# Kernel optimization log

Hardware: AMD Instinct MI355X
Metric: run time of the kernel (lower is better)

The kernel has to match this reference:

```python
import jax, jax.numpy as jnp
import numpy as np

V, C, BLK = 32000, 512, 2048
B, T = 4, 2048
EPS = 1e-5


def _layernorm(x, g, b):
    mu = jnp.mean(x, axis=-1, keepdims=True)
    var = jnp.mean(jnp.square(x - mu), axis=-1, keepdims=True)
    return (x - mu) * jax.lax.rsqrt(var + EPS) * g + b


def setup_inputs() -> dict:
    key = jax.random.key(0)
    ks = jax.random.split(key, 16)
    s = 0.02
    return {
        "idx": jax.random.randint(ks[0], (B, T), 0, V),
        "targets": jax.random.randint(ks[1], (B, T), 0, V),
        "tok_emb": jax.random.normal(ks[2], (V, C), jnp.float32) * s,
        "pos_emb": jax.random.normal(ks[3], (BLK, C), jnp.float32) * s,
        "Wk": jax.random.normal(ks[4], (C, C), jnp.float32) * s,
        "Wq": jax.random.normal(ks[5], (C, C), jnp.float32) * s,
        "Wv": jax.random.normal(ks[6], (C, C), jnp.float32) * s,
        "W1": jax.random.normal(ks[7], (4 * C, C), jnp.float32) * s,
        "b1": jnp.zeros((4 * C,), jnp.float32),
        "W2": jax.random.normal(ks[8], (C, 4 * C), jnp.float32) * s,
        "b2": jnp.zeros((C,), jnp.float32),
        "g1": jnp.ones((C,), jnp.float32),
        "beta1": jnp.zeros((C,), jnp.float32),
        "g2": jnp.ones((C,), jnp.float32),
        "beta2": jnp.zeros((C,), jnp.float32),
        "Wlm": jax.random.normal(ks[9], (V, C), jnp.float32) * s,
        "blm": jnp.zeros((V,), jnp.float32),
    }


def reference(idx, targets, tok_emb, pos_emb, Wk, Wq, Wv, W1, b1, W2, b2,
              g1, beta1, g2, beta2, Wlm, blm):
    # embeddings
    x = tok_emb[idx] + pos_emb[:T]  # [B,T,C]
    # single-head causal self-attention (dropout = identity, eval mode)
    h = _layernorm(x, g1, beta1)
    q = jnp.einsum('btc,dc->btd', h, Wq)
    k = jnp.einsum('btc,dc->btd', h, Wk)
    v = jnp.einsum('btc,dc->btd', h, Wv)
    wei = jnp.einsum('btd,bsd->bts', q, k) * (C ** -0.5)  # [B,T,T]
    mask = jnp.tril(jnp.ones((T, T), bool))
    wei = jnp.where(mask, wei, -jnp.inf)
    wei = jax.nn.softmax(wei, axis=-1)
    x = x + jnp.einsum('bts,bsd->btd', wei, v)
    # FFN
    h2 = _layernorm(x, g2, beta2)
    ff = jax.nn.relu(jnp.einsum('btc,fc->btf', h2, W1) + b1)
    x = x + jnp.einsum('btf,cf->btc', ff, W2) + b2
    # lm head + cross-entropy
    logits = (jnp.einsum('btc,vc->btv', x, Wlm) + blm).reshape(B * T, V)
    logp = jax.nn.log_softmax(logits, axis=-1)
    loss = -jnp.mean(jnp.take_along_axis(logp, targets.reshape(-1, 1), axis=1))
    return logits, loss
```

## Files before the change

### kernel.cpp

```cpp
#include <hip/hip_runtime.h>

typedef __bf16 bf16;
typedef __bf16 bf16x8 __attribute__((ext_vector_type(8)));
typedef float  f32x4  __attribute__((ext_vector_type(4)));

#define NB 4
#define NT 2048
#define NC 512
#define NV 32000
#define NROWS (NB*NT)
#define NCHUNK (NV/256)
#define LNEPS 1e-5f
#define SMEM_B 131072

static __device__ __forceinline__ void load_lds16(const bf16* g, char* l) {
  __builtin_amdgcn_global_load_lds(
      (const __attribute__((address_space(1))) void*)g,
      (__attribute__((address_space(3))) void*)l, 16, 0, 0);
}

static __device__ __forceinline__ void bar() {
  asm volatile("" ::: "memory");
  __builtin_amdgcn_s_barrier();
  asm volatile("" ::: "memory");
}

__global__ __launch_bounds__(256)
void cvt_kernel(const float* __restrict__ in, bf16* __restrict__ out, int n8) {
  long i = (long)blockIdx.x * 256 + threadIdx.x;
  long stride = (long)gridDim.x * 256;
  for (; i < n8; i += stride) {
    const float* p = in + i * 8;
    f32x4 a = *(const f32x4*)p;
    f32x4 b = *(const f32x4*)(p + 4);
    bf16x8 o;
    o[0]=(bf16)a.x; o[1]=(bf16)a.y; o[2]=(bf16)a.z; o[3]=(bf16)a.w;
    o[4]=(bf16)b.x; o[5]=(bf16)b.y; o[6]=(bf16)b.z; o[7]=(bf16)b.w;
    *(bf16x8*)(out + i*8) = o;
  }
}

__global__ __launch_bounds__(64)
void embed_ln_kernel(const int* __restrict__ idx, const float* __restrict__ tok,
                     const float* __restrict__ pos, const float* __restrict__ gw,
                     const float* __restrict__ bw,
                     float* __restrict__ x0, bf16* __restrict__ h1) {
  int row = blockIdx.x;
  int t = row & (NT-1);
  int id = idx[row];
  int lane = threadIdx.x;
  const float* tr = tok + (long)id*NC + lane*8;
  const float* pr = pos + (long)t*NC + lane*8;
  f32x4 a0 = *(const f32x4*)tr, a1 = *(const f32x4*)(tr+4);
  f32x4 p0 = *(const f32x4*)pr, p1 = *(const f32x4*)(pr+4);
  f32x4 r0 = a0 + p0, r1 = a1 + p1;
  float* o = x0 + (long)row*NC + lane*8;
  *(f32x4*)o = r0; *(f32x4*)(o+4) = r1;
  float v[8] = {r0.x,r0.y,r0.z,r0.w,r1.x,r1.y,r1.z,r1.w};
  float s = 0.f;
  #pragma unroll
  for (int j=0;j<8;++j) s += v[j];
  #pragma unroll
  for (int m=32;m>=1;m>>=1) s += __shfl_xor(s, m);
  float mu = s * (1.f/NC);
  float sq = 0.f;
  #pragma unroll
  for (int j=0;j<8;++j) { v[j] -= mu; sq += v[j]*v[j]; }
  #pragma unroll
  for (int m=32;m>=1;m>>=1) sq += __shfl_xor(sq, m);
  float rs = rsqrtf(sq * (1.f/NC) + LNEPS);
  const float* gp = gw + lane*8;
  const float* bp = bw + lane*8;
  f32x4 g0 = *(const f32x4*)gp, g1 = *(const f32x4*)(gp+4);
  f32x4 b0 = *(const f32x4*)bp, b1 = *(const f32x4*)(bp+4);
  float gg[8] = {g0.x,g0.y,g0.z,g0.w,g1.x,g1.y,g1.z,g1.w};
  float bb[8] = {b0.x,b0.y,b0.z,b0.w,b1.x,b1.y,b1.z,b1.w};
  bf16x8 oo;
  #pragma unroll
  for (int j=0;j<8;++j) oo[j] = (bf16)(v[j]*rs*gg[j] + bb[j]);
  *(bf16x8*)(h1 + (long)row*NC + lane*8) = oo;
}

__global__ __launch_bounds__(64)
void ln_kernel(const float* __restrict__ x, const float* __restrict__ gw,
               const float* __restrict__ bw, bf16* __restrict__ out) {
  int row = blockIdx.x;
  int lane = threadIdx.x;
  const float* xr = x + (long)row*NC + lane*8;
  f32x4 a = *(const f32x4*)xr;
  f32x4 b = *(const f32x4*)(xr+4);
  float v[8] = {a.x,a.y,a.z,a.w,b.x,b.y,b.z,b.w};
  float s = 0.f;
  #pragma unroll
  for (int j=0;j<8;++j) s += v[j];
  #pragma unroll
  for (int m=32;m>=1;m>>=1) s += __shfl_xor(s, m);
  float mu = s * (1.f/NC);
  float sq = 0.f;
  #pragma unroll
  for (int j=0;j<8;++j) { v[j] -= mu; sq += v[j]*v[j]; }
  #pragma unroll
  for (int m=32;m>=1;m>>=1) sq += __shfl_xor(sq, m);
  float rs = rsqrtf(sq * (1.f/NC) + LNEPS);
  const float* gp = gw + lane*8;
  const float* bp = bw + lane*8;
  f32x4 g0 = *(const f32x4*)gp, g1 = *(const f32x4*)(gp+4);
  f32x4 b0 = *(const f32x4*)bp, b1 = *(const f32x4*)(bp+4);
  float gg[8] = {g0.x,g0.y,g0.z,g0.w,g1.x,g1.y,g1.z,g1.w};
  float bb[8] = {b0.x,b0.y,b0.z,b0.w,b1.x,b1.y,b1.z,b1.w};
  bf16x8 o;
  #pragma unroll
  for (int j=0;j<8;++j) o[j] = (bf16)(v[j]*rs*gg[j] + bb[j]);
  *(bf16x8*)(out + (long)row*NC + lane*8) = o;
}

__global__ __launch_bounds__(256)
void transpose_kernel(const bf16* __restrict__ v, long ldv, bf16* __restrict__ vt) {
  __shared__ bf16 tile[64][66];
  int b = blockIdx.z;
  int t0 = blockIdx.x*64, c0 = blockIdx.y*64;
  int tid = threadIdx.x;
  int r = tid >> 2, ch = (tid & 3) * 16;
  const bf16* src = v + ((long)b*NT + t0 + r)*ldv + c0 + ch;
  #pragma unroll
  for (int i=0;i<16;++i) tile[r][ch+i] = src[i];
  __syncthreads();
  bf16x8 o0, o1;
  #pragma unroll
  for (int i=0;i<8;++i) o0[i] = tile[ch+i][r];
  #pragma unroll
  for (int i=0;i<8;++i) o1[i] = tile[ch+8+i][r];
  bf16* dst = vt + ((long)b*NC + c0 + r)*NT + t0 + ch;
  *(bf16x8*)dst = o0;
  *(bf16x8*)(dst+8) = o1;
}

__global__ __launch_bounds__(256)
void softmax_kernel(float* __restrict__ S) {
  const int row = blockIdx.x;
  const int t = row & (NT-1);
  const int tid = threadIdx.x;
  float* sr = S + (long)row*NT;
  bf16* pr = (bf16*)S + (long)row*(2*NT);
  const float scale = 0.044194173824159216f;
  f32x4 v0 = *(const f32x4*)(sr + tid*8);
  f32x4 v1 = *(const f32x4*)(sr + tid*8 + 4);
  float v[8] = {v0.x,v0.y,v0.z,v0.w,v1.x,v1.y,v1.z,v1.w};
  int cb = tid*8;
  float mx = -1e30f;
  #pragma unroll
  for (int j=0;j<8;++j) {
    v[j] = (cb + j <= t) ? v[j]*scale : -1e30f;
    mx = fmaxf(mx, v[j]);
  }
  __shared__ float redm[4];
  #pragma unroll
  for (int m=32;m>=1;m>>=1) mx = fmaxf(mx, __shfl_xor(mx, m));
  if ((tid & 63) == 0) redm[tid>>6] = mx;
  __syncthreads();
  mx = fmaxf(fmaxf(redm[0],redm[1]), fmaxf(redm[2],redm[3]));
  float e[8]; float s = 0.f;
  #pragma unroll
  for (int j=0;j<8;++j) { e[j] = (cb + j <= t) ? __expf(v[j]-mx) : 0.f; s += e[j]; }
  __shared__ float reds[4];
  #pragma unroll
  for (int m=32;m>=1;m>>=1) s += __shfl_xor(s, m);
  if ((tid & 63) == 0) reds[tid>>6] = s;
  __syncthreads();
  s = reds[0]+reds[1]+reds[2]+reds[3];
  float inv = 1.f/s;
  bf16x8 o;
  #pragma unroll
  for (int j=0;j<8;++j) o[j] = (bf16)(e[j]*inv);
  *(bf16x8*)(pr + cb) = o;
}

enum { EPI_F32=0, EPI_BF16=1, EPI_BIAS_RELU_BF16=2, EPI_BIAS_RES_BF16=3, EPI_RES_F32=4, EPI_LMHEAD=5 };

template<int EPI, bool CAUSAL=false, bool KLIMIT=false, bool SWAP=false>
__global__ __launch_bounds__(512,2)
void gemm256(const bf16* __restrict__ A, const bf16* __restrict__ B, int nkt,
             long lda, long ldb, long sAb, long sBb,
             float* __restrict__ outf, bf16* __restrict__ outb, long ldo, long sOb,
             const float* __restrict__ bias,
             const float* __restrict__ res, long ldr, long sRb,
             float* __restrict__ pmax, float* __restrict__ psum) {
  extern __shared__ char smem[];
  int bn, bm;
  if constexpr (SWAP) { bm = blockIdx.x; bn = blockIdx.y; }
  else               { bn = blockIdx.x; bm = blockIdx.y; }
  const int bz = blockIdx.z;
  if constexpr (CAUSAL) { if (bn > bm) return; }
  int nkt_eff = nkt;
  if constexpr (KLIMIT) { int c = (bm+1)*4; if (c < nkt_eff) nkt_eff = c; }

  const int tid = threadIdx.x;
  const int wid = tid >> 6, lane = tid & 63;
  const int wr = wid >> 2, wc = wid & 3;
  const int l15 = lane & 15, g = lane >> 4;

  const bf16* Ab = A + (long)bz*sAb + (long)bm*256*lda;
  const bf16* Bb = B + (long)bz*sBb + (long)bn*256*ldb;

  const int colsw = 8 * ((tid & 7) ^ ((tid >> 3) & 7));
  const bf16* A0 = Ab + (long)(tid >> 3)*lda + colsw;
  const bf16* B0 = Bb + (long)(tid >> 3)*ldb + colsw;

  auto stage = [&](int ab, int t, int h, int slot) {
    char* dst = smem + slot*65536 + ab*32768 + h*16384 + wid*1024;
    const bf16* s0 = (ab ? B0 : A0) + (long)(h*128)*(ab ? ldb : lda) + (long)t*64;
    load_lds16(s0, dst);
    load_lds16(s0 + 64*(ab ? ldb : lda), dst + 8192);
  };

  const char* sm = smem;
  auto aLoad = [&](int slot, int m, int kk) -> bf16x8 {
    int row = m*16 + l15;
    int b = row*128 + ((kk*64 + g*16) ^ ((row & 7) << 4));
    return *(const bf16x8*)(sm + slot*65536 + wr*16384 + b);
  };
  auto bLoad = [&](int slot, int n, int kk) -> bf16x8 {
    int row = (wc & 1)*64 + n*16 + l15;
    int b = row*128 + ((kk*64 + g*16) ^ ((row & 7) << 4));
    return *(const bf16x8*)(sm + slot*65536 + 32768 + (wc >> 1)*16384 + b);
  };

  f32x4 acc[8][4] = {};

  stage(0, 0, 0, 0);
  stage(0, 0, 1, 0);
  stage(1, 0, 0, 0);
  stage(1, 0, 1, 0);
  stage(0, 1, 0, 1);
  asm volatile("s_waitcnt vmcnt(2)" ::: "memory");
  bar();

  const int niter = nkt_eff >> 1;
  for (int it = 0; it < niter; ++it) {
    const int t0 = 2*it, t1 = 2*it + 1;
    const int tn0 = (t0+2 < nkt_eff) ? t0+2 : nkt_eff-1;
    const int tn1 = (t1+2 < nkt_eff) ? t1+2 : nkt_eff-1;
    bf16x8 a0[4][2], a1[4][2], b0[2][2], b1[2][2];

    #pragma unroll
    for (int m=0;m<4;++m) { a0[m][0]=aLoad(0,m,0); a0[m][1]=aLoad(0,m,1); }
    #pragma unroll
    for (int n=0;n<2;++n) { b0[n][0]=bLoad(0,n,0); b0[n][1]=bLoad(0,n,1); }
    stage(0, t1, 1, 1);
    bar();
    __builtin_amdgcn_s_setprio(1);
    #pragma unroll
    for (int m=0;m<4;++m)
      #pragma unroll
      for (int n=0;n<2;++n) {
        acc[m][n] = __builtin_amdgcn_mfma_f32_16x16x32_bf16(a0[m][0], b0[n][0], acc[m][n],0,0,0);
        acc[m][n] = __builtin_amdgcn_mfma_f32_16x16x32_bf16(a0[m][1], b0[n][1], acc[m][n],0,0,0);
      }
    __builtin_amdgcn_s_setprio(0);
    bar();

    #pragma unroll
    for (int n=0;n<2;++n) { b1[n][0]=bLoad(0,n+2,0); b1[n][1]=bLoad(0,n+2,1); }
    stage(1, t1, 0, 1);
    bar();
    __builtin_amdgcn_s_setprio(1);
    #pragma unroll
    for (int m=0;m<4;++m)
      #pragma unroll
      for (int n=0;n<2;++n) {
        acc[m][n+2] = __builtin_amdgcn_mfma_f32_16x16x32_bf16(a0[m][0], b1[n][0], acc[m][n+2],0,0,0);
        acc[m][n+2] = __builtin_amdgcn_mfma_f32_16x16x32_bf16(a0[m][1], b1[n][1], acc[m][n+2],0,0,0);
      }
    __builtin_amdgcn_s_setprio(0);
    bar();

    #pragma unroll
    for (int m=0;m<4;++m) { a1[m][0]=aLoad(0,m+4,0); a1[m][1]=aLoad(0,m+4,1); }
    stage(1, t1, 1, 1);
    bar();
    __builtin_amdgcn_s_setprio(1);
    #pragma unroll
    for (int m=0;m<4;++m)
      #pragma unroll
      for (int n=0;n<2;++n) {
        acc[m+4][n+2] = __builtin_amdgcn_mfma_f32_16x16x32_bf16(a1[m][0], b1[n][0], acc[m+4][n+2],0,0,0);
        acc[m+4][n+2] = __builtin_amdgcn_mfma_f32_16x16x32_bf16(a1[m][1], b1[n][1], acc[m+4][n+2],0,0,0);
      }
    __builtin_amdgcn_s_setprio(0);
    bar();

    stage(0, tn0, 0, 0);
    asm volatile("s_waitcnt vmcnt(2)" ::: "memory");
    bar();
    __builtin_amdgcn_s_setprio(1);
    #pragma unroll
    for (int m=0;m<4;++m)
      #pragma unroll
      for (int n=0;n<2;++n) {
        acc[m+4][n] = __builtin_amdgcn_mfma_f32_16x16x32_bf16(a1[m][0], b0[n][0], acc[m+4][n],0,0,0);
        acc[m+4][n] = __builtin_amdgcn_mfma_f32_16x16x32_bf16(a1[m][1], b0[n][1], acc[m+4][n],0,0,0);
      }
    __builtin_amdgcn_s_setprio(0);
    bar();

    #pragma unroll
    for (int m=0;m<4;++m) { a0[m][0]=aLoad(1,m,0); a0[m][1]=aLoad(1,m,1); }
    #pragma unroll
    for (int n=0;n<2;++n) { b0[n][0]=bLoad(1,n,0); b0[n][1]=bLoad(1,n,1); }
    stage(0, tn0, 1, 0);
    bar();
    __builtin_amdgcn_s_setprio(1);
    #pragma unroll
    for (int m=0;m<4;++m)
      #pragma unroll
      for (int n=0;n<2;++n) {
        acc[m][n] = __builtin_amdgcn_mfma_f32_16x16x32_bf16(a0[m][0], b0[n][0], acc[m][n],0,0,0);
        acc[m][n] = __builtin_amdgcn_mfma_f32_16x16x32_bf16(a0[m][1], b0[n][1], acc[m][n],0,0,0);
      }
    __builtin_amdgcn_s_setprio(0);
    bar();

    #pragma unroll
    for (int n=0;n<2;++n) { b1[n][0]=bLoad(1,n+2,0); b1[n][1]=bLoad(1,n+2,1); }
    stage(1, tn0, 0, 0);
    bar();
    __builtin_amdgcn_s_setprio(1);
    #pragma unroll
    for (int m=0;m<4;++m)
      #pragma unroll
      for (int n=0;n<2;++n) {
        acc[m][n+2] = __builtin_amdgcn_mfma_f32_16x16x32_bf16(a0[m][0], b1[n][0], acc[m][n+2],0,0,0);
        acc[m][n+2] = __builtin_amdgcn_mfma_f32_16x16x32_bf16(a0[m][1], b1[n][1], acc[m][n+2],0,0,0);
      }
    __builtin_amdgcn_s_setprio(0);
    bar();

    #pragma unroll
    for (int m=0;m<4;++m) { a1[m][0]=aLoad(1,m+4,0); a1[m][1]=aLoad(1,m+4,1); }
    stage(1, tn0, 1, 0);
    bar();
    __builtin_amdgcn_s_setprio(1);
    #pragma unroll
    for (int m=0;m<4;++m)
      #pragma unroll
      for (int n=0;n<2;++n) {
        acc[m+4][n+2] = __builtin_amdgcn_mfma_f32_16x16x32_bf16(a1[m][0], b1[n][0], acc[m+4][n+2],0,0,0);
        acc[m+4][n+2] = __builtin_amdgcn_mfma_f32_16x16x32_bf16(a1[m][1], b1[n][1], acc[m+4][n+2],0,0,0);
      }
    __builtin_amdgcn_s_setprio(0);
    bar();

    stage(0, tn1, 0, 1);
    asm volatile("s_waitcnt vmcnt(2)" ::: "memory");
    bar();
    __builtin_amdgcn_s_setprio(1);
    #pragma unroll
    for (int m=0;m<4;++m)
      #pragma unroll
      for (int n=0;n<2;++n) {
        acc[m+4][n] = __builtin_amdgcn_mfma_f32_16x16x32_bf16(a1[m][0], b0[n][0], acc[m+4][n],0,0,0);
        acc[m+4][n] = __builtin_amdgcn_mfma_f32_16x16x32_bf16(a1[m][1], b0[n][1], acc[m+4][n],0,0,0);
      }
    __builtin_amdgcn_s_setprio(0);
    bar();
  }

  const long rowbase = (long)bm*256 + wr*128;
  const long colbase = (long)bn*256 + wc*64;

  if constexpr (EPI == EPI_LMHEAD) {
    #pragma unroll
    for (int m=0;m<8;++m)
      #pragma unroll
      for (int n=0;n<4;++n) {
        long c = colbase + n*16 + l15;
        float bv = bias[c];
        #pragma unroll
        for (int q_=0;q_<4;++q_) {
          acc[m][n][q_] += bv;
          long rr = rowbase + m*16 + g*4 + q_;
          __builtin_nontemporal_store(acc[m][n][q_], &outf[rr*ldo + c]);
        }
      }
    __syncthreads();
    float* redm = (float*)smem;
    float* reds = redm + 1024;
    #pragma unroll
    for (int m=0;m<8;++m)
      #pragma unroll
      for (int q_=0;q_<4;++q_) {
        float mx = fmaxf(fmaxf(acc[m][0][q_], acc[m][1][q_]),
                         fmaxf(acc[m][2][q_], acc[m][3][q_]));
        #pragma unroll
        for (int msk=8;msk>=1;msk>>=1) mx = fmaxf(mx, __shfl_xor(mx, msk));
        float se = 0.f;
        #pragma unroll
        for (int n=0;n<4;++n) se += __expf(acc[m][n][q_] - mx);
        #pragma unroll
        for (int msk=8;msk>=1;msk>>=1) se += __shfl_xor(se, msk);
        if (l15 == 0) {
          int rloc = wr*128 + m*16 + g*4 + q_;
          redm[wc*256 + rloc] = mx;
          reds[wc*256 + rloc] = se;
        }
      }
    __syncthreads();
    if (tid < 256) {
      float m0=redm[tid], m1=redm[256+tid], m2=redm[512+tid], m3=redm[768+tid];
      float M = fmaxf(fmaxf(m0,m1), fmaxf(m2,m3));
      float Sv = reds[tid]*__expf(m0-M) + reds[256+tid]*__expf(m1-M)
               + reds[512+tid]*__expf(m2-M) + reds[768+tid]*__expf(m3-M);
      long row = (long)bm*256 + tid;
      pmax[row*NCHUNK + bn] = M;
      psum[row*NCHUNK + bn] = Sv;
    }
  } else {
    #pragma unroll
    for (int m=0;m<8;++m)
      #pragma unroll
      for (int n=0;n<4;++n) {
        long c = colbase + n*16 + l15;
        #pragma unroll
        for (int q_=0;q_<4;++q_) {
          long rr = rowbase + m*16 + g*4 + q_;
          float v = acc[m][n][q_];
          if constexpr (EPI == EPI_F32) {
            outf[(long)bz*sOb + rr*ldo + c] = v;
          } else if constexpr (EPI == EPI_BF16) {
            outb[(long)bz*sOb + rr*ldo + c] = (bf16)v;
          } else if constexpr (EPI == EPI_BIAS_RELU_BF16) {
            outb[rr*ldo + c] = (bf16)fmaxf(v + bias[c], 0.f);
          } else if constexpr (EPI == EPI_BIAS_RES_BF16) {
            outb[rr*ldo + c] = (bf16)(v + bias[c] + res[rr*ldr + c]);
          } else if constexpr (EPI == EPI_RES_F32) {
            outf[(long)bz*sOb + rr*ldo + c] = v + res[(long)bz*sRb + rr*ldr + c];
          }
        }
      }
  }
}

__global__ __launch_bounds__(256)
void loss1_kernel(const float* __restrict__ pmax, const float* __restrict__ psum,
                  const float* __restrict__ logits, const int* __restrict__ targets,
                  float* __restrict__ rowloss) {
  int row = blockIdx.x;
  int tid = threadIdx.x;
  int lane = tid & 63, wv = tid >> 6;
  float cm = (tid < NCHUNK) ? pmax[(long)row*NCHUNK + tid] : -1e30f;
  float cs = (tid < NCHUNK) ? psum[(long)row*NCHUNK + tid] : 0.f;
  float mx = cm;
  #pragma unroll
  for (int m=32;m>=1;m>>=1) mx = fmaxf(mx, __shfl_xor(mx, m));
  __shared__ float rm[4];
  if (lane == 0) rm[wv] = mx;
  __syncthreads();
  float M = fmaxf(fmaxf(rm[0],rm[1]), fmaxf(rm[2],rm[3]));
  float sc = cs * __expf(cm - M);
  #pragma unroll
  for (int m=32;m>=1;m>>=1) sc += __shfl_xor(sc, m);
  __shared__ float rs_[4];
  if (lane == 0) rs_[wv] = sc;
  __syncthreads();
  if (tid == 0) {
    float Sv = rs_[0]+rs_[1]+rs_[2]+rs_[3];
    float lse = M + logf(Sv);
    int tgt = targets[row];
    float lg = logits[(long)row*NV + tgt];
    rowloss[row] = lse - lg;
  }
}

__global__ __launch_bounds__(256)
void loss2_kernel(const float* __restrict__ rowloss, float* __restrict__ out) {
  int tid = threadIdx.x;
  float s = 0.f;
  for (int i = tid; i < NROWS; i += 256) s += rowloss[i];
  #pragma unroll
  for (int m=32;m>=1;m>>=1) s += __shfl_xor(s, m);
  __shared__ float rs_[4];
  if ((tid & 63) == 0) rs_[tid>>6] = s;
  __syncthreads();
  if (tid == 0) out[0] = (rs_[0]+rs_[1]+rs_[2]+rs_[3]) * (1.f/NROWS);
}

extern "C" void kernel_launch(void* const* d_in, const int* in_sizes, int n_in,
                              void* d_out, int out_size, void* d_ws, size_t ws_size,
                              hipStream_t stream) {
  const int*   idx  = (const int*)d_in[0];
  const int*   tgt  = (const int*)d_in[1];
  const float* tok  = (const float*)d_in[2];
  const float* pos  = (const float*)d_in[3];
  const float* Wk   = (const float*)d_in[4];
  const float* Wq   = (const float*)d_in[5];
  const float* Wv   = (const float*)d_in[6];
  const float* W1   = (const float*)d_in[7];
  const float* b1   = (const float*)d_in[8];
  const float* W2   = (const float*)d_in[9];
  const float* b2   = (const float*)d_in[10];
  const float* g1   = (const float*)d_in[11];
  const float* be1  = (const float*)d_in[12];
  const float* g2   = (const float*)d_in[13];
  const float* be2  = (const float*)d_in[14];
  const float* Wlm  = (const float*)d_in[15];
  const float* blm  = (const float*)d_in[16];

  float* logits = (float*)d_out;
  float* loss   = logits + (long)NROWS*NV;

  char* w = (char*)d_ws;
  auto alloc = [&](size_t bytes) -> char* {
    char* p = w; w += (bytes + 255) & ~(size_t)255; return p;
  };
  bf16* wqkvb = (bf16*)alloc((size_t)3*NC*NC*2);
  bf16* w1b   = (bf16*)alloc((size_t)4*NC*NC*2);
  bf16* w2b   = (bf16*)alloc((size_t)4*NC*NC*2);
  bf16* wlmb  = (bf16*)alloc((size_t)NV*NC*2);
  float* x0   = (float*)alloc((size_t)NROWS*NC*4);
  bf16* h1b   = (bf16*)alloc((size_t)NROWS*NC*2);
  bf16* qkvb  = (bf16*)alloc((size_t)NROWS*3*NC*2);
  bf16* vtb   = (bf16*)alloc((size_t)NROWS*NC*2);
  float* Sb   = (float*)alloc((size_t)NB*NT*NT*4);
  float* x1   = (float*)alloc((size_t)NROWS*NC*4);
  bf16* h2b   = (bf16*)alloc((size_t)NROWS*NC*2);
  bf16* ffb   = (bf16*)alloc((size_t)NROWS*4*NC*2);
  bf16* x2b   = (bf16*)alloc((size_t)NROWS*NC*2);
  float* pmax = (float*)alloc((size_t)NROWS*NCHUNK*4);
  float* psum = (float*)alloc((size_t)NROWS*NCHUNK*4);
  float* rowloss = (float*)alloc((size_t)NROWS*4);

  hipFuncSetAttribute((const void*)gemm256<EPI_BF16,false,false,false>,
                      hipFuncAttributeMaxDynamicSharedMemorySize, SMEM_B);
  hipFuncSetAttribute((const void*)gemm256<EPI_F32,true,false,false>,
                      hipFuncAttributeMaxDynamicSharedMemorySize, SMEM_B);
  hipFuncSetAttribute((const void*)gemm256<EPI_RES_F32,false,true,false>,
                      hipFuncAttributeMaxDynamicSharedMemorySize, SMEM_B);
  hipFuncSetAttribute((const void*)gemm256<EPI_BIAS_RELU_BF16,false,false,true>,
                      hipFuncAttributeMaxDynamicSharedMemorySize, SMEM_B);
  hipFuncSetAttribute((const void*)gemm256<EPI_BIAS_RES_BF16,false,false,false>,
                      hipFuncAttributeMaxDynamicSharedMemorySize, SMEM_B);
  hipFuncSetAttribute((const void*)gemm256<EPI_LMHEAD,false,false,true>,
                      hipFuncAttributeMaxDynamicSharedMemorySize, SMEM_B);

  auto cvt = [&](const float* in, bf16* out, long n) {
    int n8 = (int)(n/8);
    int blocks = (n8 + 255)/256; if (blocks > 2048) blocks = 2048;
    cvt_kernel<<<blocks, 256, 0, stream>>>(in, out, n8);
  };
  cvt(Wq, wqkvb, (long)NC*NC);
  cvt(Wk, wqkvb + (long)NC*NC, (long)NC*NC);
  cvt(Wv, wqkvb + (long)2*NC*NC, (long)NC*NC);
  cvt(W1, w1b, (long)4*NC*NC);
  cvt(W2, w2b, (long)4*NC*NC);
  cvt(Wlm, wlmb, (long)NV*NC);

  embed_ln_kernel<<<NROWS, 64, 0, stream>>>(idx, tok, pos, g1, be1, x0, h1b);

  gemm256<EPI_BF16><<<dim3(6,32,1), 512, SMEM_B, stream>>>(
      h1b, wqkvb, 8, NC, NC, 0, 0, nullptr, qkvb, 3*NC, 0,
      nullptr, nullptr, 0, 0, nullptr, nullptr);

  transpose_kernel<<<dim3(NT/64, NC/64, NB), 256, 0, stream>>>(qkvb + 2*NC, 3*NC, vtb);

  gemm256<EPI_F32,true><<<dim3(8,8,NB), 512, SMEM_B, stream>>>(
      qkvb, qkvb + NC, 8, 3*NC, 3*NC, (long)NT*3*NC, (long)NT*3*NC,
      Sb, nullptr, NT, (long)NT*NT,
      nullptr, nullptr, 0, 0, nullptr, nullptr);

  softmax_kernel<<<NROWS, 256, 0, stream>>>(Sb);

  gemm256<EPI_RES_F32,false,true><<<dim3(2,8,NB), 512, SMEM_B, stream>>>(
      (const bf16*)Sb, vtb, 32, 2*NT, NT, (long)NT*2*NT, (long)NC*NT,
      x1, nullptr, NC, (long)NT*NC,
      nullptr, x0, NC, (long)NT*NC, nullptr, nullptr);

  ln_kernel<<<NROWS, 64, 0, stream>>>(x1, g2, be2, h2b);

  gemm256<EPI_BIAS_RELU_BF16,false,false,true><<<dim3(32,8,1), 512, SMEM_B, stream>>>(
      h2b, w1b, 8, NC, NC, 0, 0, nullptr, ffb, 4*NC, 0,
      b1, nullptr, 0, 0, nullptr, nullptr);

  gemm256<EPI_BIAS_RES_BF16><<<dim3(2,32,1), 512, SMEM_B, stream>>>(
      ffb, w2b, 32, 4*NC, 4*NC, 0, 0, nullptr, x2b, NC, 0,
      b2, x1, NC, 0, nullptr, nullptr);

  gemm256<EPI_LMHEAD,false,false,true><<<dim3(32,NCHUNK,1), 512, SMEM_B, stream>>>(
      x2b, wlmb, 8, NC, NC, 0, 0, logits, nullptr, NV, 0,
      blm, nullptr, 0, 0, pmax, psum);

  loss1_kernel<<<NROWS, 256, 0, stream>>>(pmax, psum, logits, tgt, rowloss);
  loss2_kernel<<<1, 256, 0, stream>>>(rowloss, loss);
}
```

Baseline: 774.1 us.

## Split-K the PV and FFN2 GEMMs and make the LM head persistent

The PV GEMM is split along K into 512-wide chunks, so its grid grows from 64 to 256 blocks while causal limits are kept per chunk. A new kernel sums the partials with the residual and applies LayerNorm 2 in one pass. FFN2 is likewise split into 4 K-chunks whose fp32 partials are reduced together with the bias and residual. The LM head moves to a persistent kernel of 256 blocks, each keeping its A row tile and walking several vocabulary panels with a continuous prefetch pipeline. This targets the underfilled grids and the per-tile prologue cost, and pays for it with extra fp32 partial traffic and additional reduction kernels.

```diff
diff --git a/kernel.cpp b/kernel.cpp
--- a/kernel.cpp
+++ b/kernel.cpp
@@ -12,6 +12,7 @@
 #define NCHUNK (NV/256)
 #define LNEPS 1e-5f
 #define SMEM_B 131072
+#define SMEM_LM (131072 + 8192)
 
 static __device__ __forceinline__ void load_lds16(const bf16* g, char* l) {
   __builtin_amdgcn_global_load_lds(
@@ -81,39 +82,6 @@
   *(bf16x8*)(h1 + (long)row*NC + lane*8) = oo;
 }
 
-__global__ __launch_bounds__(64)
-void ln_kernel(const float* __restrict__ x, const float* __restrict__ gw,
-               const float* __restrict__ bw, bf16* __restrict__ out) {
-  int row = blockIdx.x;
-  int lane = threadIdx.x;
-  const float* xr = x + (long)row*NC + lane*8;
-  f32x4 a = *(const f32x4*)xr;
-  f32x4 b = *(const f32x4*)(xr+4);
-  float v[8] = {a.x,a.y,a.z,a.w,b.x,b.y,b.z,b.w};
-  float s = 0.f;
-  #pragma unroll
-  for (int j=0;j<8;++j) s += v[j];
-  #pragma unroll
-  for (int m=32;m>=1;m>>=1) s += __shfl_xor(s, m);
-  float mu = s * (1.f/NC);
-  float sq = 0.f;
-  #pragma unroll
-  for (int j=0;j<8;++j) { v[j] -= mu; sq += v[j]*v[j]; }
-  #pragma unroll
-  for (int m=32;m>=1;m>>=1) sq += __shfl_xor(sq, m);
-  float rs = rsqrtf(sq * (1.f/NC) + LNEPS);
-  const float* gp = gw + lane*8;
-  const float* bp = bw + lane*8;
-  f32x4 g0 = *(const f32x4*)gp, g1 = *(const f32x4*)(gp+4);
-  f32x4 b0 = *(const f32x4*)bp, b1 = *(const f32x4*)(bp+4);
-  float gg[8] = {g0.x,g0.y,g0.z,g0.w,g1.x,g1.y,g1.z,g1.w};
-  float bb[8] = {b0.x,b0.y,b0.z,b0.w,b1.x,b1.y,b1.z,b1.w};
-  bf16x8 o;
-  #pragma unroll
-  for (int j=0;j<8;++j) o[j] = (bf16)(v[j]*rs*gg[j] + bb[j]);
-  *(bf16x8*)(out + (long)row*NC + lane*8) = o;
-}
-
 __global__ __launch_bounds__(256)
 void transpose_kernel(const bf16* __restrict__ v, long ldv, bf16* __restrict__ vt) {
   __shared__ bf16 tile[64][66];
@@ -175,16 +143,15 @@
   *(bf16x8*)(pr + cb) = o;
 }
 
-enum { EPI_F32=0, EPI_BF16=1, EPI_BIAS_RELU_BF16=2, EPI_BIAS_RES_BF16=3, EPI_RES_F32=4, EPI_LMHEAD=5 };
-
-template<int EPI, bool CAUSAL=false, bool KLIMIT=false, bool SWAP=false>
+enum { EPI_F32=0, EPI_BF16=1, EPI_BIAS_RELU_BF16=2, EPI_BIAS_RES_BF16=3, EPI_RES_F32=4 };
+
+template<int EPI, bool CAUSAL=false, bool SWAP=false, bool KCHUNK=false>
 __global__ __launch_bounds__(512,2)
 void gemm256(const bf16* __restrict__ A, const bf16* __restrict__ B, int nkt,
              long lda, long ldb, long sAb, long sBb,
              float* __restrict__ outf, bf16* __restrict__ outb, long ldo, long sOb,
              const float* __restrict__ bias,
-             const float* __restrict__ res, long ldr, long sRb,
-             float* __restrict__ pmax, float* __restrict__ psum) {
+             const float* __restrict__ res, long ldr, long sRb) {
   extern __shared__ char smem[];
   int bn, bm;
   if constexpr (SWAP) { bm = blockIdx.x; bn = blockIdx.y; }
@@ -192,15 +159,23 @@
   const int bz = blockIdx.z;
   if constexpr (CAUSAL) { if (bn > bm) return; }
   int nkt_eff = nkt;
-  if constexpr (KLIMIT) { int c = (bm+1)*4; if (c < nkt_eff) nkt_eff = c; }
+  int bzAB = bz;
+  long kOff = 0;
+  if constexpr (KCHUNK) {
+    int c = bz >> 2; bzAB = bz & 3;
+    int lim = (bm+1)*4 - c*8;
+    if (lim <= 0) return;
+    if (lim < nkt_eff) nkt_eff = lim;
+    kOff = (long)c*512;
+  }
 
   const int tid = threadIdx.x;
   const int wid = tid >> 6, lane = tid & 63;
   const int wr = wid >> 2, wc = wid & 3;
   const int l15 = lane & 15, g = lane >> 4;
 
-  const bf16* Ab = A + (long)bz*sAb + (long)bm*256*lda;
-  const bf16* Bb = B + (long)bz*sBb + (long)bn*256*ldb;
+  const bf16* Ab = A + (long)bzAB*sAb + kOff + (long)bm*256*lda;
+  const bf16* Bb = B + (long)bzAB*sBb + kOff + (long)bn*256*ldb;
 
   const int colsw = 8 * ((tid & 7) ^ ((tid >> 3) & 7));
   const bf16* A0 = Ab + (long)(tid >> 3)*lda + colsw;
@@ -258,7 +233,6 @@
       }
     __builtin_amdgcn_s_setprio(0);
     bar();
-
     #pragma unroll
     for (int n=0;n<2;++n) { b1[n][0]=bLoad(0,n+2,0); b1[n][1]=bLoad(0,n+2,1); }
     stage(1, t1, 0, 1);
@@ -273,7 +247,6 @@
       }
     __builtin_amdgcn_s_setprio(0);
     bar();
-
     #pragma unroll
     for (int m=0;m<4;++m) { a1[m][0]=aLoad(0,m+4,0); a1[m][1]=aLoad(0,m+4,1); }
     stage(1, t1, 1, 1);
@@ -288,7 +261,6 @@
       }
     __builtin_amdgcn_s_setprio(0);
     bar();
-
     stage(0, tn0, 0, 0);
     asm volatile("s_waitcnt vmcnt(2)" ::: "memory");
     bar();
@@ -302,7 +274,6 @@
       }
     __builtin_amdgcn_s_setprio(0);
     bar();
-
     #pragma unroll
     for (int m=0;m<4;++m) { a0[m][0]=aLoad(1,m,0); a0[m][1]=aLoad(1,m,1); }
     #pragma unroll
@@ -319,7 +290,6 @@
       }
     __builtin_amdgcn_s_setprio(0);
     bar();
-
     #pragma unroll
     for (int n=0;n<2;++n) { b1[n][0]=bLoad(1,n+2,0); b1[n][1]=bLoad(1,n+2,1); }
     stage(1, tn0, 0, 0);
@@ -334,7 +304,6 @@
       }
     __builtin_amdgcn_s_setprio(0);
     bar();
-
     #pragma unroll
     for (int m=0;m<4;++m) { a1[m][0]=aLoad(1,m+4,0); a1[m][1]=aLoad(1,m+4,1); }
     stage(1, tn0, 1, 0);
@@ -349,7 +318,6 @@
       }
     __builtin_amdgcn_s_setprio(0);
     bar();
-
     stage(0, tn1, 0, 1);
     asm volatile("s_waitcnt vmcnt(2)" ::: "memory");
     bar();
@@ -368,76 +336,327 @@
   const long rowbase = (long)bm*256 + wr*128;
   const long colbase = (long)bn*256 + wc*64;
 
-  if constexpr (EPI == EPI_LMHEAD) {
-    #pragma unroll
-    for (int m=0;m<8;++m)
-      #pragma unroll
-      for (int n=0;n<4;++n) {
-        long c = colbase + n*16 + l15;
-        float bv = bias[c];
+  #pragma unroll
+  for (int m=0;m<8;++m)
+    #pragma unroll
+    for (int n=0;n<4;++n) {
+      long c = colbase + n*16 + l15;
+      #pragma unroll
+      for (int q_=0;q_<4;++q_) {
+        long rr = rowbase + m*16 + g*4 + q_;
+        float v = acc[m][n][q_];
+        if constexpr (EPI == EPI_F32) {
+          outf[(long)bz*sOb + rr*ldo + c] = v;
+        } else if constexpr (EPI == EPI_BF16) {
+          outb[(long)bz*sOb + rr*ldo + c] = (bf16)v;
+        } else if constexpr (EPI == EPI_BIAS_RELU_BF16) {
+          outb[rr*ldo + c] = (bf16)fmaxf(v + bias[c], 0.f);
+        } else if constexpr (EPI == EPI_BIAS_RES_BF16) {
+          outb[rr*ldo + c] = (bf16)(v + bias[c] + res[rr*ldr + c]);
+        } else if constexpr (EPI == EPI_RES_F32) {
+          outf[(long)bz*sOb + rr*ldo + c] = v + res[(long)bz*sRb + rr*ldr + c];
+        }
+      }
+    }
+}
+
+__global__ __launch_bounds__(512,2)
+void lmhead_kernel(const bf16* __restrict__ A, const bf16* __restrict__ B,
+                   const float* __restrict__ bias, float* __restrict__ outf,
+                   float* __restrict__ pmax, float* __restrict__ psum) {
+  extern __shared__ char smem[];
+  float* redm = (float*)(smem + 131072);
+  float* reds = redm + 1024;
+  const int blk = blockIdx.x;
+  const int grp = blk & 7;
+  const int bm  = blk >> 3;
+  const int npan = (grp < 5) ? 16 : 15;
+  const long lda = NC, ldb = NC, ldo = NV;
+
+  const int tid = threadIdx.x;
+  const int wid = tid >> 6, lane = tid & 63;
+  const int wr = wid >> 2, wc = wid & 3;
+  const int l15 = lane & 15, g = lane >> 4;
+
+  const int colsw = 8 * ((tid & 7) ^ ((tid >> 3) & 7));
+  const bf16* A0 = A + (long)bm*256*lda + (long)(tid >> 3)*lda + colsw;
+  const bf16* B0 = B + (long)(tid >> 3)*ldb + colsw;
+
+  auto stage = [&](int ab, int gt, int h, int slot) {
+    char* dst = smem + slot*65536 + ab*32768 + h*16384 + wid*1024;
+    const bf16* s0;
+    if (ab) {
+      int panel = gt >> 3, k = gt & 7;
+      s0 = B0 + ((long)(grp + 8*panel)*256 + h*128)*ldb + k*64;
+    } else {
+      int k = gt & 7;
+      s0 = A0 + (long)(h*128)*lda + k*64;
+    }
+    load_lds16(s0, dst);
+    load_lds16(s0 + 64*(ab ? ldb : lda), dst + 8192);
+  };
+
+  const char* sm = smem;
+  auto aLoad = [&](int slot, int m, int kk) -> bf16x8 {
+    int row = m*16 + l15;
+    int b = row*128 + ((kk*64 + g*16) ^ ((row & 7) << 4));
+    return *(const bf16x8*)(sm + slot*65536 + wr*16384 + b);
+  };
+  auto bLoad = [&](int slot, int n, int kk) -> bf16x8 {
+    int row = (wc & 1)*64 + n*16 + l15;
+    int b = row*128 + ((kk*64 + g*16) ^ ((row & 7) << 4));
+    return *(const bf16x8*)(sm + slot*65536 + 32768 + (wc >> 1)*16384 + b);
+  };
+
+  f32x4 acc[8][4] = {};
+
+  stage(0, 0, 0, 0);
+  stage(0, 0, 1, 0);
+  stage(1, 0, 0, 0);
+  stage(1, 0, 1, 0);
+  stage(0, 1, 0, 1);
+  asm volatile("s_waitcnt vmcnt(2)" ::: "memory");
+  bar();
+
+  const int ntile = npan*8;
+  const int niter = ntile >> 1;
+  for (int it = 0; it < niter; ++it) {
+    const int t0 = 2*it, t1 = 2*it + 1;
+    const int tn0 = (t0+2 < ntile) ? t0+2 : ntile-1;
+    const int tn1 = (t1+2 < ntile) ? t1+2 : ntile-1;
+    bf16x8 a0[4][2], a1[4][2], b0[2][2], b1[2][2];
+
+    #pragma unroll
+    for (int m=0;m<4;++m) { a0[m][0]=aLoad(0,m,0); a0[m][1]=aLoad(0,m,1); }
+    #pragma unroll
+    for (int n=0;n<2;++n) { b0[n][0]=bLoad(0,n,0); b0[n][1]=bLoad(0,n,1); }
+    stage(0, t1, 1, 1);
+    bar();
+    __builtin_amdgcn_s_setprio(1);
+    #pragma unroll
+    for (int m=0;m<4;++m)
+      #pragma unroll
+      for (int n=0;n<2;++n) {
+        acc[m][n] = __builtin_amdgcn_mfma_f32_16x16x32_bf16(a0[m][0], b0[n][0], acc[m][n],0,0,0);
+        acc[m][n] = __builtin_amdgcn_mfma_f32_16x16x32_bf16(a0[m][1], b0[n][1], acc[m][n],0,0,0);
+      }
+    __builtin_amdgcn_s_setprio(0);
+    bar();
+    #pragma unroll
+    for (int n=0;n<2;++n) { b1[n][0]=bLoad(0,n+2,0); b1[n][1]=bLoad(0,n+2,1); }
+    stage(1, t1, 0, 1);
+    bar();
+    __builtin_amdgcn_s_setprio(1);
+    #pragma unroll
+    for (int m=0;m<4;++m)
+      #pragma unroll
+      for (int n=0;n<2;++n) {
+        acc[m][n+2] = __builtin_amdgcn_mfma_f32_16x16x32_bf16(a0[m][0], b1[n][0], acc[m][n+2],0,0,0);
+        acc[m][n+2] = __builtin_amdgcn_mfma_f32_16x16x32_bf16(a0[m][1], b1[n][1], acc[m][n+2],0,0,0);
+      }
+    __builtin_amdgcn_s_setprio(0);
+    bar();
+    #pragma unroll
+    for (int m=0;m<4;++m) { a1[m][0]=aLoad(0,m+4,0); a1[m][1]=aLoad(0,m+4,1); }
+    stage(1, t1, 1, 1);
+    bar();
+    __builtin_amdgcn_s_setprio(1);
+    #pragma unroll
+    for (int m=0;m<4;++m)
+      #pragma unroll
+      for (int n=0;n<2;++n) {
+        acc[m+4][n+2] = __builtin_amdgcn_mfma_f32_16x16x32_bf16(a1[m][0], b1[n][0], acc[m+4][n+2],0,0,0);
+        acc[m+4][n+2] = __builtin_amdgcn_mfma_f32_16x16x32_bf16(a1[m][1], b1[n][1], acc[m+4][n+2],0,0,0);
+      }
+    __builtin_amdgcn_s_setprio(0);
+    bar();
+    stage(0, tn0, 0, 0);
+    asm volatile("s_waitcnt vmcnt(2)" ::: "memory");
+    bar();
+    __builtin_amdgcn_s_setprio(1);
+    #pragma unroll
+    for (int m=0;m<4;++m)
+      #pragma unroll
+      for (int n=0;n<2;++n) {
+        acc[m+4][n] = __builtin_amdgcn_mfma_f32_16x16x32_bf16(a1[m][0], b0[n][0], acc[m+4][n],0,0,0);
+        acc[m+4][n] = __builtin_amdgcn_mfma_f32_16x16x32_bf16(a1[m][1], b0[n][1], acc[m+4][n],0,0,0);
+      }
+    __builtin_amdgcn_s_setprio(0);
+    bar();
+    #pragma unroll
+    for (int m=0;m<4;++m) { a0[m][0]=aLoad(1,m,0); a0[m][1]=aLoad(1,m,1); }
+    #pragma unroll
+    for (int n=0;n<2;++n) { b0[n][0]=bLoad(1,n,0); b0[n][1]=bLoad(1,n,1); }
+    stage(0, tn0, 1, 0);
+    bar();
+    __builtin_amdgcn_s_setprio(1);
+    #pragma unroll
+    for (int m=0;m<4;++m)
+      #pragma unroll
+      for (int n=0;n<2;++n) {
+        acc[m][n] = __builtin_amdgcn_mfma_f32_16x16x32_bf16(a0[m][0], b0[n][0], acc[m][n],0,0,0);
+        acc[m][n] = __builtin_amdgcn_mfma_f32_16x16x32_bf16(a0[m][1], b0[n][1], acc[m][n],0,0,0);
+      }
+    __builtin_amdgcn_s_setprio(0);
+    bar();
+    #pragma unroll
+    for (int n=0;n<2;++n) { b1[n][0]=bLoad(1,n+2,0); b1[n][1]=bLoad(1,n+2,1); }
+    stage(1, tn0, 0, 0);
+    bar();
+    __builtin_amdgcn_s_setprio(1);
+    #pragma unroll
+    for (int m=0;m<4;++m)
+      #pragma unroll
+      for (int n=0;n<2;++n) {
+        acc[m][n+2] = __builtin_amdgcn_mfma_f32_16x16x32_bf16(a0[m][0], b1[n][0], acc[m][n+2],0,0,0);
+        acc[m][n+2] = __builtin_amdgcn_mfma_f32_16x16x32_bf16(a0[m][1], b1[n][1], acc[m][n+2],0,0,0);
+      }
+    __builtin_amdgcn_s_setprio(0);
+    bar();
+    #pragma unroll
+    for (int m=0;m<4;++m) { a1[m][0]=aLoad(1,m+4,0); a1[m][1]=aLoad(1,m+4,1); }
+    stage(1, tn0, 1, 0);
+    bar();
+    __builtin_amdgcn_s_setprio(1);
+    #pragma unroll
+    for (int m=0;m<4;++m)
+      #pragma unroll
+      for (int n=0;n<2;++n) {
+        acc[m+4][n+2] = __builtin_amdgcn_mfma_f32_16x16x32_bf16(a1[m][0], b1[n][0], acc[m+4][n+2],0,0,0);
+        acc[m+4][n+2] = __builtin_amdgcn_mfma_f32_16x16x32_bf16(a1[m][1], b1[n][1], acc[m+4][n+2],0,0,0);
+      }
+    __builtin_amdgcn_s_setprio(0);
+    bar();
+    stage(0, tn1, 0, 1);
+    asm volatile("s_waitcnt vmcnt(2)" ::: "memory");
+    bar();
+    __builtin_amdgcn_s_setprio(1);
+    #pragma unroll
+    for (int m=0;m<4;++m)
+      #pragma unroll
+      for (int n=0;n<2;++n) {
+        acc[m+4][n] = __builtin_amdgcn_mfma_f32_16x16x32_bf16(a1[m][0], b0[n][0], acc[m+4][n],0,0,0);
+        acc[m+4][n] = __builtin_amdgcn_mfma_f32_16x16x32_bf16(a1[m][1], b0[n][1], acc[m+4][n],0,0,0);
+      }
+    __builtin_amdgcn_s_setprio(0);
+    bar();
+
+    if ((it & 3) == 3) {
+      const int bn = grp + 8*(it >> 2);
+      const long rowb = (long)bm*256 + wr*128;
+      const long colb = (long)bn*256 + wc*64;
+      #pragma unroll
+      for (int m=0;m<8;++m)
+        #pragma unroll
+        for (int n=0;n<4;++n) {
+          long c = colb + n*16 + l15;
+          float bv = bias[c];
+          #pragma unroll
+          for (int q_=0;q_<4;++q_) {
+            acc[m][n][q_] += bv;
+            long rr = rowb + m*16 + g*4 + q_;
+            __builtin_nontemporal_store(acc[m][n][q_], &outf[rr*ldo + c]);
+          }
+        }
+      #pragma unroll
+      for (int m=0;m<8;++m)
         #pragma unroll
         for (int q_=0;q_<4;++q_) {
-          acc[m][n][q_] += bv;
-          long rr = rowbase + m*16 + g*4 + q_;
-          __builtin_nontemporal_store(acc[m][n][q_], &outf[rr*ldo + c]);
-        }
-      }
-    __syncthreads();
-    float* redm = (float*)smem;
-    float* reds = redm + 1024;
-    #pragma unroll
-    for (int m=0;m<8;++m)
-      #pragma unroll
-      for (int q_=0;q_<4;++q_) {
-        float mx = fmaxf(fmaxf(acc[m][0][q_], acc[m][1][q_]),
-                         fmaxf(acc[m][2][q_], acc[m][3][q_]));
-        #pragma unroll
-        for (int msk=8;msk>=1;msk>>=1) mx = fmaxf(mx, __shfl_xor(mx, msk));
-        float se = 0.f;
-        #pragma unroll
-        for (int n=0;n<4;++n) se += __expf(acc[m][n][q_] - mx);
-        #pragma unroll
-        for (int msk=8;msk>=1;msk>>=1) se += __shfl_xor(se, msk);
-        if (l15 == 0) {
-          int rloc = wr*128 + m*16 + g*4 + q_;
-          redm[wc*256 + rloc] = mx;
-          reds[wc*256 + rloc] = se;
-        }
-      }
-    __syncthreads();
-    if (tid < 256) {
-      float m0=redm[tid], m1=redm[256+tid], m2=redm[512+tid], m3=redm[768+tid];
-      float M = fmaxf(fmaxf(m0,m1), fmaxf(m2,m3));
-      float Sv = reds[tid]*__expf(m0-M) + reds[256+tid]*__expf(m1-M)
-               + reds[512+tid]*__expf(m2-M) + reds[768+tid]*__expf(m3-M);
-      long row = (long)bm*256 + tid;
-      pmax[row*NCHUNK + bn] = M;
-      psum[row*NCHUNK + bn] = Sv;
-    }
-  } else {
-    #pragma unroll
-    for (int m=0;m<8;++m)
-      #pragma unroll
-      for (int n=0;n<4;++n) {
-        long c = colbase + n*16 + l15;
-        #pragma unroll
-        for (int q_=0;q_<4;++q_) {
-          long rr = rowbase + m*16 + g*4 + q_;
-          float v = acc[m][n][q_];
-          if constexpr (EPI == EPI_F32) {
-            outf[(long)bz*sOb + rr*ldo + c] = v;
-          } else if constexpr (EPI == EPI_BF16) {
-            outb[(long)bz*sOb + rr*ldo + c] = (bf16)v;
-          } else if constexpr (EPI == EPI_BIAS_RELU_BF16) {
-            outb[rr*ldo + c] = (bf16)fmaxf(v + bias[c], 0.f);
-          } else if constexpr (EPI == EPI_BIAS_RES_BF16) {
-            outb[rr*ldo + c] = (bf16)(v + bias[c] + res[rr*ldr + c]);
-          } else if constexpr (EPI == EPI_RES_F32) {
-            outf[(long)bz*sOb + rr*ldo + c] = v + res[(long)bz*sRb + rr*ldr + c];
+          float mx = fmaxf(fmaxf(acc[m][0][q_], acc[m][1][q_]),
+                           fmaxf(acc[m][2][q_], acc[m][3][q_]));
+          #pragma unroll
+          for (int msk=8;msk>=1;msk>>=1) mx = fmaxf(mx, __shfl_xor(mx, msk));
+          float se = 0.f;
+          #pragma unroll
+          for (int n=0;n<4;++n) se += __expf(acc[m][n][q_] - mx);
+          #pragma unroll
+          for (int msk=8;msk>=1;msk>>=1) se += __shfl_xor(se, msk);
+          if (l15 == 0) {
+            int rl = wr*128 + m*16 + g*4 + q_;
+            redm[wc*256 + rl] = mx;
+            reds[wc*256 + rl] = se;
           }
         }
-      }
+      __syncthreads();
+      if (tid < 256) {
+        float m0=redm[tid], m1=redm[256+tid], m2=redm[512+tid], m3=redm[768+tid];
+        float M = fmaxf(fmaxf(m0,m1), fmaxf(m2,m3));
+        float Sv = reds[tid]*__expf(m0-M) + reds[256+tid]*__expf(m1-M)
+                 + reds[512+tid]*__expf(m2-M) + reds[768+tid]*__expf(m3-M);
+        long row = (long)bm*256 + tid;
+        pmax[row*NCHUNK + bn] = M;
+        psum[row*NCHUNK + bn] = Sv;
+      }
+      __syncthreads();
+      #pragma unroll
+      for (int m=0;m<8;++m)
+        #pragma unroll
+        for (int n=0;n<4;++n)
+          #pragma unroll
+          for (int q_=0;q_<4;++q_) acc[m][n][q_] = 0.f;
+    }
   }
+}
+
+__global__ __launch_bounds__(64)
+void pv_combine_ln_kernel(const float* __restrict__ part, const float* __restrict__ x0,
+                          const float* __restrict__ gw, const float* __restrict__ bw,
+                          float* __restrict__ x1, bf16* __restrict__ h2) {
+  int row = blockIdx.x;
+  int b = row >> 11, t = row & (NT-1);
+  int lane = threadIdx.x;
+  int nC = (t >> 9) + 1;
+  const float* xr = x0 + (long)row*NC + lane*8;
+  f32x4 a0 = *(const f32x4*)xr, a1 = *(const f32x4*)(xr+4);
+  for (int c = 0; c < nC; ++c) {
+    const float* pr = part + ((long)(c*4 + b)*NT + t)*NC + lane*8;
+    a0 += *(const f32x4*)pr; a1 += *(const f32x4*)(pr+4);
+  }
+  float* o = x1 + (long)row*NC + lane*8;
+  *(f32x4*)o = a0; *(f32x4*)(o+4) = a1;
+  float v[8] = {a0.x,a0.y,a0.z,a0.w,a1.x,a1.y,a1.z,a1.w};
+  float s = 0.f;
+  #pragma unroll
+  for (int j=0;j<8;++j) s += v[j];
+  #pragma unroll
+  for (int m=32;m>=1;m>>=1) s += __shfl_xor(s, m);
+  float mu = s * (1.f/NC);
+  float sq = 0.f;
+  #pragma unroll
+  for (int j=0;j<8;++j) { v[j] -= mu; sq += v[j]*v[j]; }
+  #pragma unroll
+  for (int m=32;m>=1;m>>=1) sq += __shfl_xor(sq, m);
+  float rs = rsqrtf(sq * (1.f/NC) + LNEPS);
+  const float* gp = gw + lane*8;
+  const float* bp = bw + lane*8;
+  f32x4 g0 = *(const f32x4*)gp, g1 = *(const f32x4*)(gp+4);
+  f32x4 b0 = *(const f32x4*)bp, b1 = *(const f32x4*)(bp+4);
+  float gg[8] = {g0.x,g0.y,g0.z,g0.w,g1.x,g1.y,g1.z,g1.w};
+  float bb[8] = {b0.x,b0.y,b0.z,b0.w,b1.x,b1.y,b1.z,b1.w};
+  bf16x8 oo;
+  #pragma unroll
+  for (int j=0;j<8;++j) oo[j] = (bf16)(v[j]*rs*gg[j] + bb[j]);
+  *(bf16x8*)(h2 + (long)row*NC + lane*8) = oo;
+}
+
+__global__ __launch_bounds__(64)
+void ffn2_combine_kernel(const float* __restrict__ part, const float* __restrict__ x1,
+                         const float* __restrict__ b2, bf16* __restrict__ x2) {
+  int row = blockIdx.x;
+  int lane = threadIdx.x;
+  const float* xr = x1 + (long)row*NC + lane*8;
+  f32x4 a0 = *(const f32x4*)xr, a1 = *(const f32x4*)(xr+4);
+  const float* br = b2 + lane*8;
+  a0 += *(const f32x4*)br; a1 += *(const f32x4*)(br+4);
+  #pragma unroll
+  for (int z = 0; z < 4; ++z) {
+    const float* pr = part + ((long)z*NROWS + row)*NC + lane*8;
+    a0 += *(const f32x4*)pr; a1 += *(const f32x4*)(pr+4);
+  }
+  bf16x8 o;
+  o[0]=(bf16)a0.x; o[1]=(bf16)a0.y; o[2]=(bf16)a0.z; o[3]=(bf16)a0.w;
+  o[4]=(bf16)a1.x; o[5]=(bf16)a1.y; o[6]=(bf16)a1.z; o[7]=(bf16)a1.w;
+  *(bf16x8*)(x2 + (long)row*NC + lane*8) = o;
 }
 
 __global__ __launch_bounds__(256)
@@ -521,6 +740,7 @@
   bf16* qkvb  = (bf16*)alloc((size_t)NROWS*3*NC*2);
   bf16* vtb   = (bf16*)alloc((size_t)NROWS*NC*2);
   float* Sb   = (float*)alloc((size_t)NB*NT*NT*4);
+  float* pvp  = (float*)alloc((size_t)16*NT*NC*4);
   float* x1   = (float*)alloc((size_t)NROWS*NC*4);
   bf16* h2b   = (bf16*)alloc((size_t)NROWS*NC*2);
   bf16* ffb   = (bf16*)alloc((size_t)NROWS*4*NC*2);
@@ -528,19 +748,20 @@
   float* pmax = (float*)alloc((size_t)NROWS*NCHUNK*4);
   float* psum = (float*)alloc((size_t)NROWS*NCHUNK*4);
   float* rowloss = (float*)alloc((size_t)NROWS*4);
+  float* ff2p = Sb;
 
   hipFuncSetAttribute((const void*)gemm256<EPI_BF16,false,false,false>,
                       hipFuncAttributeMaxDynamicSharedMemorySize, SMEM_B);
   hipFuncSetAttribute((const void*)gemm256<EPI_F32,true,false,false>,
                       hipFuncAttributeMaxDynamicSharedMemorySize, SMEM_B);
-  hipFuncSetAttribute((const void*)gemm256<EPI_RES_F32,false,true,false>,
+  hipFuncSetAttribute((const void*)gemm256<EPI_F32,false,false,true>,
                       hipFuncAttributeMaxDynamicSharedMemorySize, SMEM_B);
-  hipFuncSetAttribute((const void*)gemm256<EPI_BIAS_RELU_BF16,false,false,true>,
+  hipFuncSetAttribute((const void*)gemm256<EPI_F32,false,false,false>,
                       hipFuncAttributeMaxDynamicSharedMemorySize, SMEM_B);
-  hipFuncSetAttribute((const void*)gemm256<EPI_BIAS_RES_BF16,false,false,false>,
+  hipFuncSetAttribute((const void*)gemm256<EPI_BIAS_RELU_BF16,false,true,false>,
                       hipFuncAttributeMaxDynamicSharedMemorySize, SMEM_B);
-  hipFuncSetAttribute((const void*)gemm256<EPI_LMHEAD,false,false,true>,
-                      hipFuncAttributeMaxDynamicSharedMemorySize, SMEM_B);
+  hipFuncSetAttribute((const void*)lmhead_kernel,
+                      hipFuncAttributeMaxDynamicSharedMemorySize, SMEM_LM);
 
   auto cvt = [&](const float* in, bf16* out, long n) {
     int n8 = (int)(n/8);
@@ -558,35 +779,36 @@
 
   gemm256<EPI_BF16><<<dim3(6,32,1), 512, SMEM_B, stream>>>(
       h1b, wqkvb, 8, NC, NC, 0, 0, nullptr, qkvb, 3*NC, 0,
-      nullptr, nullptr, 0, 0, nullptr, nullptr);
+      nullptr, nullptr, 0, 0);
 
   transpose_kernel<<<dim3(NT/64, NC/64, NB), 256, 0, stream>>>(qkvb + 2*NC, 3*NC, vtb);
 
   gemm256<EPI_F32,true><<<dim3(8,8,NB), 512, SMEM_B, stream>>>(
       qkvb, qkvb + NC, 8, 3*NC, 3*NC, (long)NT*3*NC, (long)NT*3*NC,
       Sb, nullptr, NT, (long)NT*NT,
-      nullptr, nullptr, 0, 0, nullptr, nullptr);
+      nullptr, nullptr, 0, 0);
 
   softmax_kernel<<<NROWS, 256, 0, stream>>>(Sb);
 
-  gemm256<EPI_RES_F32,false,true><<<dim3(2,8,NB), 512, SMEM_B, stream>>>(
-      (const bf16*)Sb, vtb, 32, 2*NT, NT, (long)NT*2*NT, (long)NC*NT,
-      x1, nullptr, NC, (long)NT*NC,
-      nullptr, x0, NC, (long)NT*NC, nullptr, nullptr);
-
-  ln_kernel<<<NROWS, 64, 0, stream>>>(x1, g2, be2, h2b);
-
-  gemm256<EPI_BIAS_RELU_BF16,false,false,true><<<dim3(32,8,1), 512, SMEM_B, stream>>>(
+  gemm256<EPI_F32,false,false,true><<<dim3(2,8,16), 512, SMEM_B, stream>>>(
+      (const bf16*)Sb, vtb, 8, 2*NT, NT, (long)NT*2*NT, (long)NC*NT,
+      pvp, nullptr, NC, (long)NT*NC,
+      nullptr, nullptr, 0, 0);
+
+  pv_combine_ln_kernel<<<NROWS, 64, 0, stream>>>(pvp, x0, g2, be2, x1, h2b);
+
+  gemm256<EPI_BIAS_RELU_BF16,false,true><<<dim3(32,8,1), 512, SMEM_B, stream>>>(
       h2b, w1b, 8, NC, NC, 0, 0, nullptr, ffb, 4*NC, 0,
-      b1, nullptr, 0, 0, nullptr, nullptr);
-
-  gemm256<EPI_BIAS_RES_BF16><<<dim3(2,32,1), 512, SMEM_B, stream>>>(
-      ffb, w2b, 32, 4*NC, 4*NC, 0, 0, nullptr, x2b, NC, 0,
-      b2, x1, NC, 0, nullptr, nullptr);
-
-  gemm256<EPI_LMHEAD,false,false,true><<<dim3(32,NCHUNK,1), 512, SMEM_B, stream>>>(
-      x2b, wlmb, 8, NC, NC, 0, 0, logits, nullptr, NV, 0,
-      blm, nullptr, 0, 0, pmax, psum);
+      b1, nullptr, 0, 0);
+
+  gemm256<EPI_F32><<<dim3(2,32,4), 512, SMEM_B, stream>>>(
+      ffb, w2b, 8, 4*NC, 4*NC, 512, 512,
+      ff2p, nullptr, NC, (long)NROWS*NC,
+      nullptr, nullptr, 0, 0);
+
+  ffn2_combine_kernel<<<NROWS, 64, 0, stream>>>(ff2p, x1, b2, x2b);
+
+  lmhead_kernel<<<256, 512, SMEM_LM, stream>>>(x2b, wlmb, blm, logits, pmax, psum);
 
   loss1_kernel<<<NROWS, 256, 0, stream>>>(pmax, psum, logits, tgt, rowloss);
   loss2_kernel<<<1, 256, 0, stream>>>(rowloss, loss);
```

New measurement: 1.085 ms. 40.1% more time.
